# Performance work log

Measured on AMD Instinct MI355X. Metric: run time of the kernel, lower is better.

The kernel has to match this reference:

```python
import jax, jax.numpy as jnp
import numpy as np

B, T, C = 4, 2048, 2048
H, KV, HD = 16, 4, 128  # n_head, n_kv_head, head_dim
G = H // KV             # query heads per kv head


def _rope(t, cos, sin):
    # t: [B, T, h, HD]; cos/sin: [T, HD//2] -> broadcast as [1, T, 1, HD//2]
    tr = t.reshape(t.shape[:-1] + (HD // 2, 2))
    t_r, t_i = tr[..., 0], tr[..., 1]
    c = cos[None, :, None, :]
    s = sin[None, :, None, :]
    o_r = t_r * c - t_i * s
    o_i = t_r * s + t_i * c
    return jnp.stack((o_r, o_i), axis=-1).reshape(t.shape)


def setup_inputs() -> dict:
    key = jax.random.key(0)
    ks = jax.random.split(key, 7)
    sc = 0.02
    return {
        "x": jax.random.normal(ks[0], (B, T, C), jnp.float32),
        "cos_freqs": jnp.cos(jnp.outer(jnp.arange(T, dtype=jnp.float32),
                                       1.0 / (10000.0 ** (jnp.arange(HD // 2, dtype=jnp.float32) * 2 / HD)))),
        "sin_freqs": jnp.sin(jnp.outer(jnp.arange(T, dtype=jnp.float32),
                                       1.0 / (10000.0 ** (jnp.arange(HD // 2, dtype=jnp.float32) * 2 / HD)))),
        "wq": jax.random.normal(ks[1], (H * HD, C), jnp.float32) * sc,
        "wk": jax.random.normal(ks[2], (KV * HD, C), jnp.float32) * sc,
        "wv": jax.random.normal(ks[3], (KV * HD, C), jnp.float32) * sc,
        "wo": jax.random.normal(ks[4], (C, H * HD), jnp.float32) * sc,
    }


def reference(x, cos_freqs, sin_freqs, wq, wk, wv, wo):
    # projections (Linear with bias=False: y = x @ W.T)
    q = (x @ wq.T).reshape(B, T, H, HD)
    k = (x @ wk.T).reshape(B, T, KV, HD)
    v = (x @ wv.T).reshape(B, T, KV, HD)
    q, k = _rope(q, cos_freqs, sin_freqs), _rope(k, cos_freqs, sin_freqs)
    # GQA attention without materializing repeated K/V: group q heads per kv head
    qg = q.reshape(B, T, KV, G, HD).transpose(0, 2, 3, 1, 4)  # [B,KV,G,T,HD]
    kh = k.transpose(0, 2, 1, 3)                              # [B,KV,T,HD]
    vh = v.transpose(0, 2, 1, 3)                              # [B,KV,T,HD]
    scale = 1.0 / jnp.sqrt(jnp.float32(HD))
    scores = jnp.einsum('bkgtd,bksd->bkgts', qg, kh) * scale  # [B,KV,G,T,T]
    mask = jnp.tril(jnp.ones((T, T), dtype=bool))
    scores = jnp.where(mask, scores, jnp.float32(-jnp.inf))
    attn = jax.nn.softmax(scores, axis=-1)
    out = jnp.einsum('bkgts,bksd->bkgtd', attn, vh)           # [B,KV,G,T,HD]
    out = out.transpose(0, 3, 1, 2, 4).reshape(B, T, H * HD)
    return out @ wo.T
```

## Files before the change

### kernel.cpp

```cpp
#include <hip/hip_runtime.h>
#include <hip/hip_bf16.h>
#include <math.h>

typedef __attribute__((ext_vector_type(8))) short short8;
typedef __attribute__((ext_vector_type(4))) float floatx4;

__device__ __forceinline__ float bf2f(unsigned short u) {
  union { unsigned int i; float f; } x; x.i = ((unsigned int)u) << 16; return x.f;
}
__device__ __forceinline__ unsigned short f2bf(float f) {
  union { float f; unsigned int i; } x; x.f = f;
  unsigned int r = x.i + 0x7FFFu + ((x.i >> 16) & 1u);
  return (unsigned short)(r >> 16);
}
__device__ __forceinline__ unsigned int pack2bf(float a, float b) {
  return (unsigned int)f2bf(a) | ((unsigned int)f2bf(b) << 16);
}
__device__ __forceinline__ void gl16(const void* g, void* l) {
  __builtin_amdgcn_global_load_lds(
      (const __attribute__((address_space(1))) unsigned int*)g,
      (__attribute__((address_space(3))) unsigned int*)l, 16, 0, 0);
}

__global__ void cvt_f32_bf16(const float* __restrict__ in, unsigned short* __restrict__ out, int n4) {
  int i = blockIdx.x * blockDim.x + threadIdx.x;
  if (i >= n4) return;
  float4 v = ((const float4*)in)[i];
  ushort4 o;
  o.x = f2bf(v.x); o.y = f2bf(v.y); o.z = f2bf(v.z); o.w = f2bf(v.w);
  ((ushort4*)out)[i] = o;
}

template<int MODE>
__global__ __launch_bounds__(512, 2) void gemm_bt(const unsigned short* __restrict__ A,
                                                  const unsigned short* __restrict__ Bw,
                                                  void* __restrict__ out0,
                                                  unsigned short* __restrict__ vtg,
                                                  int M, int N, int K, int nbx) {
  extern __shared__ unsigned short SM[];
  const int nb = gridDim.x;
  const int bid = blockIdx.x;
  const int tile = (bid & 7) * (nb >> 3) + (bid >> 3);
  const int n0 = (tile % nbx) * 256, m0 = (tile / nbx) * 256;
  const int tid = threadIdx.x;
  const int lane = tid & 63, wave = tid >> 6;
  const int wm = wave >> 2, wn = wave & 3;
  const int r = lane & 15, g = lane >> 4;
  const int swzr = (r >> 1) & 3;

  const int scg = (tid & 3) ^ ((tid >> 3) & 3);
  const unsigned short* Ag0 = A  + (size_t)(m0 + (tid >> 2)) * K + scg * 8;
  const unsigned short* Bg0 = Bw + (size_t)(n0 + (tid >> 2)) * K + scg * 8;
  const size_t K128 = (size_t)K * 128;
  char* const SMb = (char*)SM;

  const int aoff0 = (wm * 128 + r) * 32 + ((g ^ swzr) << 3);
  const int boff0 = 8192 + (wn * 64 + r) * 32 + ((g ^ swzr) << 3);

  auto STAGE_A = [&](int s, int t) {
    const size_t ko = (size_t)t << 5;
    char* dA = SMb + s * 32768 + wave * 1024;
    gl16(Ag0 + ko,        dA);
    gl16(Ag0 + K128 + ko, dA + 8192);
  };
  auto STAGE_B = [&](int s, int t) {
    const size_t ko = (size_t)t << 5;
    char* dB = SMb + s * 32768 + 16384 + wave * 1024;
    gl16(Bg0 + ko,        dB);
    gl16(Bg0 + K128 + ko, dB + 8192);
  };

  floatx4 acc[8][4] = {};
  const int NT = K >> 5;

  STAGE_A(0, 0); STAGE_B(0, 0);
  STAGE_A(1, 1); STAGE_B(1, 1);
  asm volatile("s_waitcnt vmcnt(4)" ::: "memory");
  __builtin_amdgcn_s_barrier();
  asm volatile("" ::: "memory");

  int rd = 0, st = 2;
  for (int t = 0; t < NT; ++t) {
    const unsigned short* Ls = SM + rd * 16384;
    const bool pf = (t + 2 < NT);

    short8 bfr[4], af[8];
#pragma unroll
    for (int j = 0; j < 4; ++j) bfr[j] = *(const short8*)&Ls[boff0 + j * 512];
#pragma unroll
    for (int i = 0; i < 4; ++i) af[i] = *(const short8*)&Ls[aoff0 + i * 512];
    if (pf) STAGE_A(st, t + 2);
    __builtin_amdgcn_s_barrier();
    asm volatile("" ::: "memory");
#pragma unroll
    for (int i = 4; i < 8; ++i) af[i] = *(const short8*)&Ls[aoff0 + i * 512];
    __builtin_amdgcn_s_setprio(1);
#pragma unroll
    for (int i = 0; i < 4; ++i)
#pragma unroll
      for (int j = 0; j < 4; ++j)
        acc[i][j] = __builtin_amdgcn_mfma_f32_16x16x32_bf16(af[i], bfr[j], acc[i][j], 0, 0, 0);
    __builtin_amdgcn_s_setprio(0);

    if (pf) {
      STAGE_B(st, t + 2);
      asm volatile("s_waitcnt vmcnt(4)" ::: "memory");
    } else {
      asm volatile("s_waitcnt vmcnt(0)" ::: "memory");
    }
    __builtin_amdgcn_s_barrier();
    asm volatile("" ::: "memory");
    __builtin_amdgcn_s_setprio(1);
#pragma unroll
    for (int i = 4; i < 8; ++i)
#pragma unroll
      for (int j = 0; j < 4; ++j)
        acc[i][j] = __builtin_amdgcn_mfma_f32_16x16x32_bf16(af[i], bfr[j], acc[i][j], 0, 0, 0);
    __builtin_amdgcn_s_setprio(0);

    rd = (rd == 2) ? 0 : rd + 1;
    st = (st == 2) ? 0 : st + 1;
  }

  if (MODE == 0) {
    float* SMf = (float*)SM;
    float* outp = (float*)out0;
#pragma unroll
    for (int sp = 0; sp < 4; ++sp) {
      __syncthreads();
      if (wn == sp) {
#pragma unroll
        for (int i = 0; i < 8; ++i)
#pragma unroll
          for (int j = 0; j < 4; ++j)
#pragma unroll
            for (int q = 0; q < 4; ++q)
              SMf[(wm * 128 + i * 16 + g * 4 + q) * 64 + j * 16 + r] = acc[i][j][q];
      }
      __syncthreads();
#pragma unroll
      for (int it = 0; it < 8; ++it) {
        int c = it * 512 + tid;
        int ml = c >> 4, c4 = c & 15;
        float4 v = *(float4*)&SMf[ml * 64 + c4 * 4];
        *(float4*)(outp + (size_t)(m0 + ml) * N + n0 + sp * 64 + c4 * 4) = v;
      }
    }
  } else if (n0 < 2560) {
    unsigned short* outp = (unsigned short*)out0;
#pragma unroll
    for (int sp = 0; sp < 2; ++sp) {
      __syncthreads();
      if (wm == sp) {
#pragma unroll
        for (int i = 0; i < 8; ++i)
#pragma unroll
          for (int j = 0; j < 4; ++j)
#pragma unroll
            for (int q = 0; q < 4; ++q)
              SM[(i * 16 + g * 4 + q) * 256 + wn * 64 + j * 16 + r] = f2bf(acc[i][j][q]);
      }
      __syncthreads();
#pragma unroll
      for (int it = 0; it < 8; ++it) {
        int c = it * 512 + tid;
        int ml = c >> 5, c8 = c & 31;
        short8 v = *(short8*)&SM[ml * 256 + c8 * 8];
        *(short8*)(outp + (size_t)(m0 + sp * 128 + ml) * N + n0 + c8 * 8) = v;
      }
    }
  } else {
#pragma unroll
    for (int sp = 0; sp < 8; ++sp) {
      __syncthreads();
      if (wave == sp) {
#pragma unroll
        for (int i = 0; i < 8; ++i)
#pragma unroll
          for (int j = 0; j < 4; ++j)
#pragma unroll
            for (int q = 0; q < 4; ++q) {
              int ml = i * 16 + g * 4 + q;
              int nl = j * 16 + r;
              SM[nl * 128 + (((ml >> 3) ^ (nl & 7)) << 3) + (ml & 7)] = f2bf(acc[i][j][q]);
            }
      }
      __syncthreads();
#pragma unroll
      for (int it = 0; it < 2; ++it) {
        int c = it * 512 + tid;
        int nl = c >> 4, m8 = c & 15;
        short8 v = *(short8*)&SM[nl * 128 + ((m8 ^ (nl & 7)) << 3)];
        *(short8*)(vtg + (size_t)(n0 - 2560 + (sp & 3) * 64 + nl) * 8192 + m0 + (sp >> 2) * 128 + m8 * 8) = v;
      }
    }
  }
}

__global__ void rope_inplace(unsigned short* __restrict__ t,
                             const float* __restrict__ cosf, const float* __restrict__ sinf,
                             int heads, int rowStride, int total, float scale) {
  int i = blockIdx.x * blockDim.x + threadIdx.x;
  if (i >= total) return;
  int d8 = i & 15;
  int rem = i >> 4;
  int head = rem % heads;
  int tok = rem / heads;
  int tpos = tok & 2047;
  unsigned short* p = t + (size_t)tok * rowStride + head * 128 + d8 * 8;
  short8 v = *(short8*)p;
  float4 c = *(const float4*)(cosf + (size_t)tpos * 64 + d8 * 4);
  float4 s = *(const float4*)(sinf + (size_t)tpos * 64 + d8 * 4);
  float cc[4] = {c.x, c.y, c.z, c.w};
  float ss[4] = {s.x, s.y, s.z, s.w};
  short8 o;
#pragma unroll
  for (int j = 0; j < 4; ++j) {
    float tr = bf2f((unsigned short)v[2 * j]);
    float ti = bf2f((unsigned short)v[2 * j + 1]);
    float orr = (tr * cc[j] - ti * ss[j]) * scale;
    float oi  = (tr * ss[j] + ti * cc[j]) * scale;
    o[2 * j]     = (short)f2bf(orr);
    o[2 * j + 1] = (short)f2bf(oi);
  }
  *(short8*)p = o;
}

__global__ __launch_bounds__(256, 2) void attn_fwd(const unsigned short* __restrict__ QKV,
                                                   const unsigned short* __restrict__ VT,
                                                   unsigned short* __restrict__ O) {
  constexpr int T = 2048;
  constexpr int LDQ = 3072;
  constexpr float NEG = -1e30f;
  __shared__ unsigned short Ks[2][64 * 128];
  __shared__ unsigned short Vs[2][128 * 64];
  const int gid = blockIdx.x;
  const int hb  = gid & 63;
  const int p   = gid >> 6;
  const int h = hb & 15, b = hb >> 4;
  const int kvh = h >> 2;
  const int tid = threadIdx.x, lane = tid & 63, w = tid >> 6;
  const int r = lane & 15, g = lane >> 4;
  const int rbase = (r & 3) + ((r >> 2) << 3);
  const int swzr  = (r & 3) | (((r >> 2) & 1) << 2);
  const size_t bT = (size_t)b * T;

  const unsigned short* Kgb = QKV + bT * LDQ + 2048 + kvh * 128;
  const unsigned short* Vgb = VT + (size_t)(kvh * 128) * 8192 + b * 2048;

  auto STAGE = [&](int bi, int kv0) {
#pragma unroll
    for (int t2 = 0; t2 < 4; ++t2) {
      int ck = w * 4 + t2;
      { int row = ck * 4 + (lane >> 4); int c16 = lane & 15;
        int swz = (row & 3) | (((row >> 3) & 1) << 2);
        gl16(Kgb + (size_t)(kv0 + row) * LDQ + ((c16 ^ swz) << 3),
             (char*)(&Ks[bi][0]) + ck * 1024); }
      { int row = ck * 8 + (lane >> 3); int c16 = lane & 7;
        gl16(Vgb + (size_t)row * 8192 + kv0 + ((c16 ^ (row & 7)) << 3),
             (char*)(&Vs[bi][0]) + ck * 1024); }
    }
  };

  for (int seg = 0; seg < 2; ++seg) {
    const int qb = seg ? p : 15 - p;
    const int q0 = qb * 128;

    short8 qf[2][4];
#pragma unroll
    for (int qt = 0; qt < 2; ++qt) {
      const unsigned short* qp = QKV + (bT + q0 + w * 32 + qt * 16 + r) * LDQ + h * 128;
#pragma unroll
      for (int c = 0; c < 4; ++c) qf[qt][c] = *(const short8*)(qp + c * 32 + g * 8);
    }

    floatx4 acc[8][2] = {};
    float mrun[2] = {NEG, NEG};
    float lrun[2] = {0.f, 0.f};

    const int ntiles = (q0 + 128) >> 6;
    STAGE(0, 0);
    asm volatile("s_waitcnt vmcnt(0)" ::: "memory");
    __syncthreads();

    for (int t = 0; t < ntiles; ++t) {
      const int cur = t & 1;
      const int kv0 = t << 6;
      if (t + 1 < ntiles) STAGE(cur ^ 1, (t + 1) << 6);

      if (kv0 <= q0 + w * 32 + 31) {
        floatx4 st[2][4] = {};
        __builtin_amdgcn_s_setprio(1);
#pragma unroll
        for (int c = 0; c < 4; ++c) {
          short8 kf[4];
#pragma unroll
          for (int kt = 0; kt < 4; ++kt) {
            const int row = rbase + ((kt & 1) << 2) + ((kt >> 1) << 5);
            kf[kt] = *(const short8*)&Ks[cur][row * 128 + (((g + 4 * c) ^ swzr) << 3)];
          }
#pragma unroll
          for (int qt = 0; qt < 2; ++qt)
#pragma unroll
            for (int kt = 0; kt < 4; ++kt)
              st[qt][kt] = __builtin_amdgcn_mfma_f32_16x16x32_bf16(kf[kt], qf[qt][c], st[qt][kt], 0, 0, 0);
        }
        __builtin_amdgcn_s_setprio(0);

        short8 va[2][8];
#pragma unroll
        for (int kc = 0; kc < 2; ++kc)
#pragma unroll
          for (int dt = 0; dt < 8; ++dt)
            va[kc][dt] = *(const short8*)&Vs[cur][(dt * 16 + r) * 64 + (((g + 4 * kc) ^ (r & 7)) << 3)];

#pragma unroll
        for (int qt = 0; qt < 2; ++qt) {
          const int qmin = q0 + w * 32 + qt * 16;
          const int qrow = qmin + r;
          float x[4][4];
          bool needmask = (kv0 + 64 > qmin);
#pragma unroll
          for (int kt = 0; kt < 4; ++kt) {
            const int kvb = kv0 + ((kt >> 1) << 5) + (g << 3) + ((kt & 1) << 2);
#pragma unroll
            for (int j = 0; j < 4; ++j) {
              float v = st[qt][kt][j];
              if (needmask) v = (kvb + j <= qrow) ? v : NEG;
              x[kt][j] = v;
            }
          }
          float mloc = x[0][0];
#pragma unroll
          for (int kt = 0; kt < 4; ++kt)
#pragma unroll
            for (int j = 0; j < 4; ++j) mloc = fmaxf(mloc, x[kt][j]);
          mloc = fmaxf(mloc, __shfl_xor(mloc, 16));
          mloc = fmaxf(mloc, __shfl_xor(mloc, 32));
          if (!__all(mloc <= mrun[qt] + 8.f)) {
            float mnew = fmaxf(mrun[qt], mloc);
            float al = __expf(mrun[qt] - mnew);
            mrun[qt] = mnew;
            lrun[qt] *= al;
#pragma unroll
            for (int dt = 0; dt < 8; ++dt) acc[dt][qt] *= al;
          }
          float pr[4][4], ssum = 0.f;
#pragma unroll
          for (int kt = 0; kt < 4; ++kt)
#pragma unroll
            for (int j = 0; j < 4; ++j) { pr[kt][j] = __expf(x[kt][j] - mrun[qt]); ssum += pr[kt][j]; }
          ssum += __shfl_xor(ssum, 16);
          ssum += __shfl_xor(ssum, 32);
          lrun[qt] += ssum;
          uint2 pk[4];
#pragma unroll
          for (int kt = 0; kt < 4; ++kt) {
            pk[kt].x = pack2bf(pr[kt][0], pr[kt][1]);
            pk[kt].y = pack2bf(pr[kt][2], pr[kt][3]);
          }
          __builtin_amdgcn_s_setprio(1);
#pragma unroll
          for (int kc = 0; kc < 2; ++kc) {
            union { unsigned int u[4]; short8 s; } bw;
            bw.u[0] = pk[2 * kc].x;
            bw.u[1] = pk[2 * kc].y;
            bw.u[2] = pk[2 * kc + 1].x;
            bw.u[3] = pk[2 * kc + 1].y;
#pragma unroll
            for (int dt = 0; dt < 8; ++dt)
              acc[dt][qt] = __builtin_amdgcn_mfma_f32_16x16x32_bf16(va[kc][dt], bw.s, acc[dt][qt], 0, 0, 0);
          }
          __builtin_amdgcn_s_setprio(0);
        }
      }

      asm volatile("s_waitcnt vmcnt(0)" ::: "memory");
      __syncthreads();
    }

#pragma unroll
    for (int qt = 0; qt < 2; ++qt) {
      float inv = 1.f / lrun[qt];
      unsigned short* op = O + (bT + q0 + w * 32 + qt * 16 + r) * 2048 + h * 128;
#pragma unroll
      for (int dt = 0; dt < 8; ++dt) {
        uint2 pkd;
        pkd.x = pack2bf(acc[dt][qt][0] * inv, acc[dt][qt][1] * inv);
        pkd.y = pack2bf(acc[dt][qt][2] * inv, acc[dt][qt][3] * inv);
        *(uint2*)(op + dt * 16 + g * 4) = pkd;
      }
    }
  }
}

extern "C" void kernel_launch(void* const* d_in, const int* in_sizes, int n_in,
                              void* d_out, int out_size, void* d_ws, size_t ws_size,
                              hipStream_t stream) {
  const float* x    = (const float*)d_in[0];
  const float* cosf = (const float*)d_in[1];
  const float* sinf = (const float*)d_in[2];
  const float* wq   = (const float*)d_in[3];
  const float* wk   = (const float*)d_in[4];
  const float* wv   = (const float*)d_in[5];
  const float* wo   = (const float*)d_in[6];

  unsigned short* xb   = (unsigned short*)d_ws;
  unsigned short* qkvw = xb   + 16777216;
  unsigned short* wob  = qkvw + 6291456;
  unsigned short* qkv  = wob  + 4194304;
  unsigned short* Vtg  = qkv  + 25165824;
  unsigned short* AO   = Vtg  + 4194304;

  static int _attr_once = []() {
    hipFuncSetAttribute((const void*)gemm_bt<0>, hipFuncAttributeMaxDynamicSharedMemorySize, 98304);
    hipFuncSetAttribute((const void*)gemm_bt<1>, hipFuncAttributeMaxDynamicSharedMemorySize, 98304);
    return 0;
  }();
  (void)_attr_once;

  cvt_f32_bf16<<<16384, 256, 0, stream>>>(x,  xb,  4194304);
  cvt_f32_bf16<<<4096,  256, 0, stream>>>(wq, qkvw,           1048576);
  cvt_f32_bf16<<<1024,  256, 0, stream>>>(wk, qkvw + 4194304, 262144);
  cvt_f32_bf16<<<1024,  256, 0, stream>>>(wv, qkvw + 5242880, 262144);
  cvt_f32_bf16<<<4096,  256, 0, stream>>>(wo, wob, 1048576);

  gemm_bt<1><<<384, 512, 98304, stream>>>(xb, qkvw, qkv, Vtg, 8192, 3072, 2048, 12);

  rope_inplace<<<8192, 256, 0, stream>>>(qkv,        cosf, sinf, 16, 3072, 2097152, 0.08838834764831845f);
  rope_inplace<<<2048, 256, 0, stream>>>(qkv + 2048, cosf, sinf, 4,  3072, 524288,  1.0f);

  attn_fwd<<<512, 256, 0, stream>>>(qkv, Vtg, AO);

  gemm_bt<0><<<256, 512, 98304, stream>>>(AO, wob, d_out, nullptr, 8192, 2048, 2048, 8);
}
```

Before: 369.2 us.

## Widen GEMM K-tile to 64 with double-buffered LDS and new swizzle

The bf16 GEMM now stages 64-wide K slices instead of 32. It uses two 64KB LDS stages in place of three 32KB stages, with a new 8-slot XOR swizzle for the 128-byte rows. Each iteration processes two K-halves in four MFMA phases, interleaving the prefetch of the next tile's halves. This aims to halve loop trip count and global-load issue overhead per FLOP. In exchange it adds more barriers per iteration, cuts prefetch depth from two tiles to one, and raises dynamic LDS to 128KB.

```diff
diff --git a/kernel.cpp b/kernel.cpp
--- a/kernel.cpp
+++ b/kernel.cpp
@@ -21,6 +21,7 @@
       (const __attribute__((address_space(1))) unsigned int*)g,
       (__attribute__((address_space(3))) unsigned int*)l, 16, 0, 0);
 }
+#define BARF  do { __builtin_amdgcn_s_barrier(); asm volatile("" ::: "memory"); } while (0)
 
 __global__ void cvt_f32_bf16(const float* __restrict__ in, unsigned short* __restrict__ out, int n4) {
   int i = blockIdx.x * blockDim.x + threadIdx.x;
@@ -46,54 +47,53 @@
   const int lane = tid & 63, wave = tid >> 6;
   const int wm = wave >> 2, wn = wave & 3;
   const int r = lane & 15, g = lane >> 4;
-  const int swzr = (r >> 1) & 3;
-
-  const int scg = (tid & 3) ^ ((tid >> 3) & 3);
-  const unsigned short* Ag0 = A  + (size_t)(m0 + (tid >> 2)) * K + scg * 8;
-  const unsigned short* Bg0 = Bw + (size_t)(n0 + (tid >> 2)) * K + scg * 8;
+  const int rh = r >> 1;
+  const int slot = (((r & 1) << 2) | g) ^ rh;
+
+  const int sg8 = (tid & 7) ^ ((tid >> 3) & 7);
+  const int srow = 2 * (tid >> 3) + (sg8 >> 2);
+  const int scol = (sg8 & 3) * 8;
+  const unsigned short* Agb = A  + (size_t)(m0 + srow) * K + scol;
+  const unsigned short* Bgb = Bw + (size_t)(n0 + srow) * K + scol;
   const size_t K128 = (size_t)K * 128;
   char* const SMb = (char*)SM;
 
-  const int aoff0 = (wm * 128 + r) * 32 + ((g ^ swzr) << 3);
-  const int boff0 = 8192 + (wn * 64 + r) * 32 + ((g ^ swzr) << 3);
-
-  auto STAGE_A = [&](int s, int t) {
-    const size_t ko = (size_t)t << 5;
-    char* dA = SMb + s * 32768 + wave * 1024;
-    gl16(Ag0 + ko,        dA);
-    gl16(Ag0 + K128 + ko, dA + 8192);
+  const int aob = (wm * 64 + rh) * 64 + slot * 8;
+  const int bob = 16384 + (wn * 32 + rh) * 64 + slot * 8;
+
+  auto STA = [&](int s, int t, int kh) {
+    const unsigned short* gp = Agb + ((size_t)t << 6) + kh * 32;
+    char* d = SMb + s * 65536 + kh * 16384 + wave * 1024;
+    gl16(gp,        d);
+    gl16(gp + K128, d + 8192);
   };
-  auto STAGE_B = [&](int s, int t) {
-    const size_t ko = (size_t)t << 5;
-    char* dB = SMb + s * 32768 + 16384 + wave * 1024;
-    gl16(Bg0 + ko,        dB);
-    gl16(Bg0 + K128 + ko, dB + 8192);
+  auto STB = [&](int s, int t, int kh) {
+    const unsigned short* gp = Bgb + ((size_t)t << 6) + kh * 32;
+    char* d = SMb + s * 65536 + 32768 + kh * 16384 + wave * 1024;
+    gl16(gp,        d);
+    gl16(gp + K128, d + 8192);
   };
 
   floatx4 acc[8][4] = {};
-  const int NT = K >> 5;
-
-  STAGE_A(0, 0); STAGE_B(0, 0);
-  STAGE_A(1, 1); STAGE_B(1, 1);
+  const int NT = K >> 6;
+
+  STA(0, 0, 0); STB(0, 0, 0);
+  STA(0, 0, 1); STB(0, 0, 1);
   asm volatile("s_waitcnt vmcnt(4)" ::: "memory");
-  __builtin_amdgcn_s_barrier();
-  asm volatile("" ::: "memory");
-
-  int rd = 0, st = 2;
+  BARF;
+
   for (int t = 0; t < NT; ++t) {
-    const unsigned short* Ls = SM + rd * 16384;
-    const bool pf = (t + 2 < NT);
-
-    short8 bfr[4], af[8];
-#pragma unroll
-    for (int j = 0; j < 4; ++j) bfr[j] = *(const short8*)&Ls[boff0 + j * 512];
-#pragma unroll
-    for (int i = 0; i < 4; ++i) af[i] = *(const short8*)&Ls[aoff0 + i * 512];
-    if (pf) STAGE_A(st, t + 2);
-    __builtin_amdgcn_s_barrier();
-    asm volatile("" ::: "memory");
-#pragma unroll
-    for (int i = 4; i < 8; ++i) af[i] = *(const short8*)&Ls[aoff0 + i * 512];
+    const int s = t & 1;
+    const unsigned short* Ls = SM + s * 32768;
+    const bool pf = (t + 1 < NT);
+    short8 bfr[4], af[4];
+
+#pragma unroll
+    for (int j = 0; j < 4; ++j) bfr[j] = *(const short8*)&Ls[bob + j * 512];
+#pragma unroll
+    for (int i = 0; i < 4; ++i) af[i] = *(const short8*)&Ls[aob + i * 512];
+    if (pf) STA(s ^ 1, t + 1, 0);
+    BARF;
     __builtin_amdgcn_s_setprio(1);
 #pragma unroll
     for (int i = 0; i < 4; ++i)
@@ -101,25 +101,56 @@
       for (int j = 0; j < 4; ++j)
         acc[i][j] = __builtin_amdgcn_mfma_f32_16x16x32_bf16(af[i], bfr[j], acc[i][j], 0, 0, 0);
     __builtin_amdgcn_s_setprio(0);
-
+    BARF;
+
+#pragma unroll
+    for (int i = 0; i < 4; ++i) af[i] = *(const short8*)&Ls[aob + (4 + i) * 512];
     if (pf) {
-      STAGE_B(st, t + 2);
+      STB(s ^ 1, t + 1, 0);
       asm volatile("s_waitcnt vmcnt(4)" ::: "memory");
     } else {
       asm volatile("s_waitcnt vmcnt(0)" ::: "memory");
     }
-    __builtin_amdgcn_s_barrier();
-    asm volatile("" ::: "memory");
+    BARF;
     __builtin_amdgcn_s_setprio(1);
 #pragma unroll
-    for (int i = 4; i < 8; ++i)
+    for (int i = 0; i < 4; ++i)
+#pragma unroll
+      for (int j = 0; j < 4; ++j)
+        acc[4 + i][j] = __builtin_amdgcn_mfma_f32_16x16x32_bf16(af[i], bfr[j], acc[4 + i][j], 0, 0, 0);
+    __builtin_amdgcn_s_setprio(0);
+    BARF;
+
+#pragma unroll
+    for (int j = 0; j < 4; ++j) bfr[j] = *(const short8*)&Ls[bob + 8192 + j * 512];
+#pragma unroll
+    for (int i = 0; i < 4; ++i) af[i] = *(const short8*)&Ls[aob + 8192 + i * 512];
+    if (pf) STA(s ^ 1, t + 1, 1);
+    BARF;
+    __builtin_amdgcn_s_setprio(1);
+#pragma unroll
+    for (int i = 0; i < 4; ++i)
 #pragma unroll
       for (int j = 0; j < 4; ++j)
         acc[i][j] = __builtin_amdgcn_mfma_f32_16x16x32_bf16(af[i], bfr[j], acc[i][j], 0, 0, 0);
     __builtin_amdgcn_s_setprio(0);
-
-    rd = (rd == 2) ? 0 : rd + 1;
-    st = (st == 2) ? 0 : st + 1;
+    BARF;
+
+#pragma unroll
+    for (int i = 0; i < 4; ++i) af[i] = *(const short8*)&Ls[aob + 8192 + (4 + i) * 512];
+    if (pf) {
+      STB(s ^ 1, t + 1, 1);
+      asm volatile("s_waitcnt vmcnt(4)" ::: "memory");
+    }
+    BARF;
+    __builtin_amdgcn_s_setprio(1);
+#pragma unroll
+    for (int i = 0; i < 4; ++i)
+#pragma unroll
+      for (int j = 0; j < 4; ++j)
+        acc[4 + i][j] = __builtin_amdgcn_mfma_f32_16x16x32_bf16(af[i], bfr[j], acc[4 + i][j], 0, 0, 0);
+    __builtin_amdgcn_s_setprio(0);
+    BARF;
   }
 
   if (MODE == 0) {
@@ -413,8 +444,8 @@
   unsigned short* AO   = Vtg  + 4194304;
 
   static int _attr_once = []() {
-    hipFuncSetAttribute((const void*)gemm_bt<0>, hipFuncAttributeMaxDynamicSharedMemorySize, 98304);
-    hipFuncSetAttribute((const void*)gemm_bt<1>, hipFuncAttributeMaxDynamicSharedMemorySize, 98304);
+    hipFuncSetAttribute((const void*)gemm_bt<0>, hipFuncAttributeMaxDynamicSharedMemorySize, 131072);
+    hipFuncSetAttribute((const void*)gemm_bt<1>, hipFuncAttributeMaxDynamicSharedMemorySize, 131072);
     return 0;
   }();
   (void)_attr_once;
@@ -425,12 +456,12 @@
   cvt_f32_bf16<<<1024,  256, 0, stream>>>(wv, qkvw + 5242880, 262144);
   cvt_f32_bf16<<<4096,  256, 0, stream>>>(wo, wob, 1048576);
 
-  gemm_bt<1><<<384, 512, 98304, stream>>>(xb, qkvw, qkv, Vtg, 8192, 3072, 2048, 12);
+  gemm_bt<1><<<384, 512, 131072, stream>>>(xb, qkvw, qkv, Vtg, 8192, 3072, 2048, 12);
 
   rope_inplace<<<8192, 256, 0, stream>>>(qkv,        cosf, sinf, 16, 3072, 2097152, 0.08838834764831845f);
   rope_inplace<<<2048, 256, 0, stream>>>(qkv + 2048, cosf, sinf, 4,  3072, 524288,  1.0f);
 
   attn_fwd<<<512, 256, 0, stream>>>(qkv, Vtg, AO);
 
-  gemm_bt<0><<<256, 512, 98304, stream>>>(AO, wob, d_out, nullptr, 8192, 2048, 2048, 8);
-}
+  gemm_bt<0><<<256, 512, 131072, stream>>>(AO, wob, d_out, nullptr, 8192, 2048, 2048, 8);
+}
```

Measured after the change: 371.0 us. Within noise of the previous version (+0.5%).
